# Optimization experiments

Hardware: AMD Instinct MI355X
Metric: run time of the kernel (lower is better)

Reference implementation:

```python
import jax, jax.numpy as jnp
import numpy as np

TOP_K = 700
NUM_GROUPS = 4
OUT_H, OUT_W = 256, 256  # original image size (output_shape)


def setup_inputs() -> dict:
    key = jax.random.key(0)
    k1, k2, k3 = jax.random.split(key, 3)
    B, E, H, W = 2, 8, 64, 64
    return {
        "objectness_logits": jax.random.normal(k1, (B, 1, H, W), dtype=jnp.float32),
        "mask_encodings": jax.random.normal(k2, (B, E, H, W), dtype=jnp.float32),
        "weights": jax.random.normal(k3, (B, (E + 1) * NUM_GROUPS, H, W), dtype=jnp.float32),
    }


def reference(objectness_logits, mask_encodings, weights):
    B, E, H, W = mask_encodings.shape
    K = TOP_K
    # objectness = sigmoid(logits); top-k over flattened spatial positions
    obj = jax.nn.sigmoid(objectness_logits).reshape(B, -1)  # [B, H*W]
    scores, idx = jax.lax.top_k(obj, K)                      # [B, K] each
    # gather per-instance dynamic conv weights (batch_select2d equivalent)
    w = weights.transpose(0, 2, 3, 1).reshape(B, -1, (E + 1) * NUM_GROUPS)  # [B, H*W, 36]
    w_sel = jnp.take_along_axis(w, idx[:, :, None], axis=1)                  # [B, K, 36]
    w_sel = w_sel.reshape(B, K * NUM_GROUPS, E + 1)                          # [B, K*4, E+1]
    wmat = w_sel[..., :E]   # [B, K*4, E] conv 1x1 filters
    bias = w_sel[..., E]    # [B, K*4]
    # grouped 1x1 conv with groups=B == per-batch matmul over encoding channels
    m = jnp.einsum('bke,behw->bkhw', wmat, mask_encodings) + bias[:, :, None, None]
    m = jax.nn.sigmoid(m)
    # masks[:, i::4] product over the 4 groups per instance
    m = m.reshape(B, K, NUM_GROUPS, H, W).prod(axis=2)  # [B, K, H, W]
    # bilinear upsample to output shape (torch align_corners=False == jax half-pixel)
    m = jax.image.resize(m, (B, K, OUT_H, OUT_W), method='bilinear')
    return m, scores
```

## Files before the change

kernel.cpp:

```cpp
#include <hip/hip_runtime.h>
#include <cstdint>
#include <cstddef>

#define TOPK 700
#define NPIX 4096
#define NG 4
#define NE 8
#define NW 36

__global__ __launch_bounds__(256) void topk_kernel(
    const float* __restrict__ logits,
    int* __restrict__ sel_idx,
    float* __restrict__ scores_out) {
  __shared__ __attribute__((aligned(16))) unsigned long long keys[NPIX];

  const int b   = blockIdx.x >> 6;
  const int blk = blockIdx.x & 63;
  const float* src = logits + b * NPIX;

  for (int i = threadIdx.x; i < NPIX; i += 256) {
    float x = src[i];
    float s = 1.0f / (1.0f + expf(-x));
    keys[i] = (((unsigned long long)__float_as_uint(s)) << 12)
              | (unsigned long long)(4095 - i);
  }
  __syncthreads();

  const int e = blk * 64 + (threadIdx.x >> 2);
  const int q = threadIdx.x & 3;
  const unsigned long long mykey = keys[e];

  const ulonglong2* k2 = (const ulonglong2*)keys;
  int rank = 0;
  const int base = q * 512;
  #pragma unroll 8
  for (int jj = 0; jj < 512; ++jj) {
    ulonglong2 kk = k2[base + jj];
    rank += (kk.x > mykey);
    rank += (kk.y > mykey);
  }
  rank += __shfl_xor(rank, 1);
  rank += __shfl_xor(rank, 2);

  if (q == 0 && rank < TOPK) {
    int idx = 4095 - (int)(mykey & 0xFFFULL);
    sel_idx[b * TOPK + rank]    = idx;
    scores_out[b * TOPK + rank] = __uint_as_float((unsigned)(mykey >> 12));
  }
}

__global__ __launch_bounds__(256) void mask_kernel(
    const float* __restrict__ enc,
    const float* __restrict__ weights,
    const int* __restrict__ sel_idx,
    float* __restrict__ out_m) {
  __shared__ float ws[NW];
  __shared__ __attribute__((aligned(16))) float tile[NPIX];

  const int bk  = blockIdx.x;
  const int b   = (bk >= TOPK) ? 1 : 0;
  const int tid = threadIdx.x;

  const int p = sel_idx[bk];
  if (tid < NW) ws[tid] = weights[(size_t)(b * NW + tid) * NPIX + p];
  __syncthreads();

  float wreg[NW];
  #pragma unroll
  for (int c = 0; c < NW; ++c) wreg[c] = ws[c];

  const float* eb = enc + (size_t)b * NE * NPIX;
  #pragma unroll
  for (int it = 0; it < 4; ++it) {
    int p4 = (tid + 256 * it) * 4;
    float4 ev[NE];
    #pragma unroll
    for (int ch = 0; ch < NE; ++ch)
      ev[ch] = *(const float4*)(eb + (size_t)ch * NPIX + p4);
    float4 s = make_float4(1.f, 1.f, 1.f, 1.f);
    #pragma unroll
    for (int g = 0; g < NG; ++g) {
      float zx = wreg[g * 9 + 8], zy = zx, zz = zx, zw = zx;
      #pragma unroll
      for (int ch = 0; ch < NE; ++ch) {
        float w = wreg[g * 9 + ch];
        zx = fmaf(w, ev[ch].x, zx);
        zy = fmaf(w, ev[ch].y, zy);
        zz = fmaf(w, ev[ch].z, zz);
        zw = fmaf(w, ev[ch].w, zw);
      }
      s.x *= __builtin_amdgcn_rcpf(1.f + __expf(-zx));
      s.y *= __builtin_amdgcn_rcpf(1.f + __expf(-zy));
      s.z *= __builtin_amdgcn_rcpf(1.f + __expf(-zz));
      s.w *= __builtin_amdgcn_rcpf(1.f + __expf(-zw));
    }
    *(float4*)(&tile[p4]) = s;
  }
  __syncthreads();

  const int tx = tid & 63;
  const int ty = tid >> 6;

  const int cxm = (tx > 0) ? tx - 1 : 0;
  const int cxp = (tx < 63) ? tx + 1 : 63;

  const float base_y = ty * 0.25f - 0.375f;
  const float fy0 = floorf(base_y);
  const float wy = base_y - fy0;
  const int y0base = (int)fy0;

  float* orow = out_m + (size_t)bk * 65536 + (size_t)ty * 256 + 4 * tx;

  for (int i = 0; i < 64; ++i) {
    int y0 = y0base + i;
    int y0c = (y0 > 0) ? y0 : 0;
    int y1c = (y0 + 1 < 63) ? y0 + 1 : 63;
    const float* r0 = &tile[y0c * 64];
    const float* r1 = &tile[y1c * 64];
    float am = r0[cxm], a0 = r0[tx], ap = r0[cxp];
    float bm = r1[cxm], b0 = r1[tx], bp = r1[cxp];
    float vm = fmaf(wy, bm - am, am);
    float v0 = fmaf(wy, b0 - a0, a0);
    float vp = fmaf(wy, bp - ap, ap);
    float4 o;
    o.x = vm * 0.375f + v0 * 0.625f;
    o.y = vm * 0.125f + v0 * 0.875f;
    o.z = v0 * 0.875f + vp * 0.125f;
    o.w = v0 * 0.625f + vp * 0.375f;
    *(float4*)(orow + (size_t)i * 4 * 256) = o;
  }
}

extern "C" void kernel_launch(void* const* d_in, const int* in_sizes, int n_in,
                              void* d_out, int out_size, void* d_ws, size_t ws_size,
                              hipStream_t stream) {
  const float* logits  = (const float*)d_in[0];
  const float* enc     = (const float*)d_in[1];
  const float* weights = (const float*)d_in[2];

  float* out        = (float*)d_out;
  float* out_m      = out;
  float* out_scores = out + (size_t)2 * TOPK * 256 * 256;
  int*   sel_idx    = (int*)d_ws;

  topk_kernel<<<128, 256, 0, stream>>>(logits, sel_idx, out_scores);
  mask_kernel<<<2 * TOPK, 256, 0, stream>>>(enc, weights, sel_idx, out_m);
}
```

Baseline: 452.6 us.

## Split mask kernel into four row-quarter blocks per instance with halo rows

Each instance mask is now handled by four blocks, each computing only 18 low-res rows (16 plus a clamped halo) into a smaller shared tile and writing a 64-row quarter of the upsampled output. The upsample loop also carries the previous row in registers instead of reloading it. The aim is more blocks and less shared memory per block, giving better occupancy and latency hiding for the store-bound output. The cost is recomputing the halo rows and reloading the per-instance weights in each of the four blocks.

Result: no change. 449.7 us (-0.6%).

```diff
diff --git a/kernel.cpp b/kernel.cpp
--- a/kernel.cpp
+++ b/kernel.cpp
@@ -55,9 +55,11 @@
     const int* __restrict__ sel_idx,
     float* __restrict__ out_m) {
   __shared__ float ws[NW];
-  __shared__ __attribute__((aligned(16))) float tile[NPIX];
+  __shared__ __attribute__((aligned(16))) float tile[18 * 64];
 
-  const int bk  = blockIdx.x;
+  const int blk = blockIdx.x;
+  const int bk  = blk >> 2;
+  const int qs  = blk & 3;
   const int b   = (bk >= TOPK) ? 1 : 0;
   const int tid = threadIdx.x;
 
@@ -69,32 +71,41 @@
   #pragma unroll
   for (int c = 0; c < NW; ++c) wreg[c] = ws[c];
 
+  const int row0 = qs * 16 - 1;
   const float* eb = enc + (size_t)b * NE * NPIX;
+
   #pragma unroll
-  for (int it = 0; it < 4; ++it) {
-    int p4 = (tid + 256 * it) * 4;
-    float4 ev[NE];
-    #pragma unroll
-    for (int ch = 0; ch < NE; ++ch)
-      ev[ch] = *(const float4*)(eb + (size_t)ch * NPIX + p4);
-    float4 s = make_float4(1.f, 1.f, 1.f, 1.f);
-    #pragma unroll
-    for (int g = 0; g < NG; ++g) {
-      float zx = wreg[g * 9 + 8], zy = zx, zz = zx, zw = zx;
+  for (int pass = 0; pass < 2; ++pass) {
+    if (pass == 0 || tid < 32) {
+      const int qq   = tid + pass * 256;
+      const int j    = qq >> 4;
+      const int col4 = (qq & 15) << 2;
+      const int g    = row0 + j;
+      const int gc   = (g < 0) ? 0 : ((g > 63) ? 63 : g);
+      const int src4 = gc * 64 + col4;
+      float4 ev[NE];
       #pragma unroll
-      for (int ch = 0; ch < NE; ++ch) {
-        float w = wreg[g * 9 + ch];
-        zx = fmaf(w, ev[ch].x, zx);
-        zy = fmaf(w, ev[ch].y, zy);
-        zz = fmaf(w, ev[ch].z, zz);
-        zw = fmaf(w, ev[ch].w, zw);
+      for (int ch = 0; ch < NE; ++ch)
+        ev[ch] = *(const float4*)(eb + (size_t)ch * NPIX + src4);
+      float4 s = make_float4(1.f, 1.f, 1.f, 1.f);
+      #pragma unroll
+      for (int g2 = 0; g2 < NG; ++g2) {
+        float zx = wreg[g2 * 9 + 8], zy = zx, zz = zx, zw = zx;
+        #pragma unroll
+        for (int ch = 0; ch < NE; ++ch) {
+          float w = wreg[g2 * 9 + ch];
+          zx = fmaf(w, ev[ch].x, zx);
+          zy = fmaf(w, ev[ch].y, zy);
+          zz = fmaf(w, ev[ch].z, zz);
+          zw = fmaf(w, ev[ch].w, zw);
+        }
+        s.x *= __builtin_amdgcn_rcpf(1.f + __expf(-zx));
+        s.y *= __builtin_amdgcn_rcpf(1.f + __expf(-zy));
+        s.z *= __builtin_amdgcn_rcpf(1.f + __expf(-zz));
+        s.w *= __builtin_amdgcn_rcpf(1.f + __expf(-zw));
       }
-      s.x *= __builtin_amdgcn_rcpf(1.f + __expf(-zx));
-      s.y *= __builtin_amdgcn_rcpf(1.f + __expf(-zy));
-      s.z *= __builtin_amdgcn_rcpf(1.f + __expf(-zz));
-      s.w *= __builtin_amdgcn_rcpf(1.f + __expf(-zw));
+      *(float4*)(&tile[j * 64 + col4]) = s;
     }
-    *(float4*)(&tile[p4]) = s;
   }
   __syncthreads();
 
@@ -106,18 +117,17 @@
 
   const float base_y = ty * 0.25f - 0.375f;
   const float fy0 = floorf(base_y);
-  const float wy = base_y - fy0;
-  const int y0base = (int)fy0;
+  const float wy  = base_y - fy0;
+  const int jbase = (ty < 2) ? 0 : 1;
 
-  float* orow = out_m + (size_t)bk * 65536 + (size_t)ty * 256 + 4 * tx;
+  float* orow = out_m + (size_t)bk * 65536 + (size_t)(qs * 64 + ty) * 256 + 4 * tx;
 
-  for (int i = 0; i < 64; ++i) {
-    int y0 = y0base + i;
-    int y0c = (y0 > 0) ? y0 : 0;
-    int y1c = (y0 + 1 < 63) ? y0 + 1 : 63;
-    const float* r0 = &tile[y0c * 64];
-    const float* r1 = &tile[y1c * 64];
-    float am = r0[cxm], a0 = r0[tx], ap = r0[cxp];
+  const float* r0 = &tile[jbase * 64];
+  float am = r0[cxm], a0 = r0[tx], ap = r0[cxp];
+
+  #pragma unroll 4
+  for (int i = 0; i < 16; ++i) {
+    const float* r1 = &tile[(jbase + i + 1) * 64];
     float bm = r1[cxm], b0 = r1[tx], bp = r1[cxp];
     float vm = fmaf(wy, bm - am, am);
     float v0 = fmaf(wy, b0 - a0, a0);
@@ -127,7 +137,8 @@
     o.y = vm * 0.125f + v0 * 0.875f;
     o.z = v0 * 0.875f + vp * 0.125f;
     o.w = v0 * 0.625f + vp * 0.375f;
-    *(float4*)(orow + (size_t)i * 4 * 256) = o;
+    *(float4*)(orow + (size_t)i * 1024) = o;
+    am = bm; a0 = b0; ap = bp;
   }
 }
 
@@ -144,5 +155,5 @@
   int*   sel_idx    = (int*)d_ws;
 
   topk_kernel<<<128, 256, 0, stream>>>(logits, sel_idx, out_scores);
-  mask_kernel<<<2 * TOPK, 256, 0, stream>>>(enc, weights, sel_idx, out_m);
+  mask_kernel<<<4 * 2 * TOPK, 256, 0, stream>>>(enc, weights, sel_idx, out_m);
 }
```
